# Kernel optimization log

Measured on AMD Instinct MI355X. Metric: run time of the kernel, lower is better.

## Reference

```python
import jax, jax.numpy as jnp
import numpy as np

N_NODES = 256
COND = 64
ARCH = [256, 512, 1024]
E = N_NODES * (N_NODES - 1) // 2  # 32640 upper-triangular edges
OUT = 2 * E                        # 65280 final-layer width
B = 512
CUTOFF = 0.0
TAU = 1.0


def _make_params(key, dims):
    ws, bs = [], []
    for i, (din, dout) in enumerate(zip(dims[:-1], dims[1:])):
        k = jax.random.fold_in(key, i)
        kw, kb = jax.random.split(k)
        ws.append(jax.random.normal(kw, (din, dout), jnp.float32) * 0.02)
        bs.append(jax.random.normal(kb, (dout,), jnp.float32) * 0.02)
    return ws, bs


def setup_inputs() -> dict:
    key = jax.random.key(0)
    kx, kg, kbig, ksmall = jax.random.split(key, 4)
    x = jax.random.normal(kx, (B, COND), jnp.float32)
    gumbel = jax.random.gumbel(kg, (B, E, 2), jnp.float32)
    dims = [COND] + ARCH + [OUT]
    bw, bb = _make_params(kbig, dims)
    sw, sb = _make_params(ksmall, dims)
    inp = {"x": x, "gumbel": gumbel}
    for i in range(4):
        inp[f"bw{i}"] = bw[i]; inp[f"bb{i}"] = bb[i]
        inp[f"sw{i}"] = sw[i]; inp[f"sb{i}"] = sb[i]
    return inp


def _expert_adj(x, ws, bs, gumbel):
    # MLP: relu on all but last layer
    h = x
    for w, b in zip(ws[:-1], bs[:-1]):
        h = jax.nn.relu(h @ w + b)
    logits = (h @ ws[-1] + bs[-1]).reshape(x.shape[0], E, 2)
    # hard gumbel-softmax (straight-through), tau=1
    g = (logits + gumbel) / TAU
    y_soft = jax.nn.softmax(g, axis=-1)
    y_hard = jax.nn.one_hot(jnp.argmax(g, axis=-1), 2, dtype=y_soft.dtype)
    y = y_hard + y_soft - jax.lax.stop_gradient(y_soft)
    x0 = y[:, :, 0]  # [B, E]
    iu, ju = jnp.triu_indices(N_NODES, k=1)
    adj = jnp.zeros((x.shape[0], N_NODES, N_NODES), x0.dtype)
    adj = adj.at[:, iu, ju].set(x0)
    return adj + jnp.swapaxes(adj, 1, 2)


def reference(x, gumbel,
              bw0, bb0, bw1, bb1, bw2, bb2, bw3, bb3,
              sw0, sb0, sw1, sb1, sw2, sb2, sw3, sb3):
    big_ws, big_bs = [bw0, bw1, bw2, bw3], [bb0, bb1, bb2, bb3]
    small_ws, small_bs = [sw0, sw1, sw2, sw3], [sb0, sb1, sb2, sb3]
    adj_big = _expert_adj(x, big_ws, big_bs, gumbel)
    adj_small = _expert_adj(x, small_ws, small_bs, gumbel)
    mask_big = x[:, 0] > CUTOFF  # [B]
    out = jnp.where(mask_big[:, None, None], adj_big, adj_small)
    return out
```

## Files before the change

### kernel.cpp

```cpp
#include <hip/hip_runtime.h>

#define N_NODES 256
#define COND    64
#define E_PAIRS 32640
#define OUTCOLS 65280
#define BATCH   512
#define SLOTS   576
#define D1      256
#define D2      512
#define D3      1024

typedef __attribute__((ext_vector_type(8))) short bf16x8;
typedef __attribute__((ext_vector_type(4))) float f32x4;

static __device__ __forceinline__ unsigned short f2bf(float f) {
    unsigned int u = __float_as_uint(f);
    u += 0x7FFF + ((u >> 16) & 1);
    return (unsigned short)(u >> 16);
}
static __device__ __forceinline__ float bf2f(unsigned short h) {
    return __uint_as_float(((unsigned int)h) << 16);
}

__global__ void k0_sort(const float* __restrict__ x, int* __restrict__ meta,
                        int* __restrict__ borig) {
    __shared__ int wc[9];
    int t = threadIdx.x;
    if (t < SLOTS) borig[t] = -1;
    int m = 0;
    if (t < BATCH) m = (x[t * COND] > 0.0f) ? 1 : 0;
    unsigned long long bm = __ballot(m);
    int wave = t >> 6;
    int lane = t & 63;
    int lanePre = __popcll(bm & ((1ull << lane) - 1ull));
    if (lane == 0) wc[wave] = __popcll(bm);
    __syncthreads();
    int nbig = 0, preBig = 0;
    #pragma unroll
    for (int w = 0; w < 8; ++w) {
        int c = wc[w];
        if (w < wave) preBig += c;
        nbig += c;
    }
    int S = (nbig + 63) & ~63;
    if (t < BATCH) {
        int onesBefore = preBig + lanePre;
        int slot = m ? onesBefore : (S + (t - onesBefore));
        borig[slot] = t;
    }
    if (t == 0) meta[0] = S;
}

template <bool GATHER, int K, int DOUT, bool SPLIT>
__global__ __launch_bounds__(256) void k1_gemm(
    const float* __restrict__ in,
    const float* __restrict__ wbig, const float* __restrict__ bbig,
    const float* __restrict__ wsml, const float* __restrict__ bsml,
    const int* __restrict__ meta, const int* __restrict__ borig,
    float* __restrict__ out,
    unsigned short* __restrict__ hb0, unsigned short* __restrict__ hb1,
    unsigned short* __restrict__ hb2) {
    __shared__ float hs[16][64 + 4];
    __shared__ float wt[16][64 + 4];
    int tid = threadIdx.x;
    int by = blockIdx.x;
    int bx = blockIdx.y;
    int r0 = by * 64;
    int cb = bx * 64;
    int S = meta[0];
    bool big = (r0 < S);
    const float* w = big ? wbig : wsml;
    const float* bias = big ? bbig : bsml;

    int lm = tid >> 2;
    int lq = tid & 3;
    int wk = tid >> 4;
    int wc = (tid & 15) * 4;

    int tm = tid >> 4;
    int tn = tid & 15;

    const float* hrow;
    if (GATHER) {
        int b = borig[r0 + lm];
        hrow = (b >= 0) ? &in[(size_t)b * K] : (const float*)0;
    } else {
        hrow = &in[(size_t)(r0 + lm) * K];
    }

    float acc[4][4];
    #pragma unroll
    for (int i = 0; i < 4; ++i)
        #pragma unroll
        for (int j = 0; j < 4; ++j) acc[i][j] = 0.f;

    for (int k0 = 0; k0 < K; k0 += 16) {
        float4 hv = make_float4(0.f, 0.f, 0.f, 0.f);
        if (!GATHER || hrow) hv = *(const float4*)&hrow[k0 + lq * 4];
        float4 wv = *(const float4*)&w[(size_t)(k0 + wk) * DOUT + cb + wc];
        __syncthreads();
        hs[lq * 4 + 0][lm] = hv.x;
        hs[lq * 4 + 1][lm] = hv.y;
        hs[lq * 4 + 2][lm] = hv.z;
        hs[lq * 4 + 3][lm] = hv.w;
        *(float4*)&wt[wk][wc] = wv;
        __syncthreads();
        #pragma unroll
        for (int kk = 0; kk < 16; ++kk) {
            float4 a  = *(const float4*)&hs[kk][tm * 4];
            float4 bf = *(const float4*)&wt[kk][tn * 4];
            acc[0][0] = fmaf(a.x, bf.x, acc[0][0]);
            acc[0][1] = fmaf(a.x, bf.y, acc[0][1]);
            acc[0][2] = fmaf(a.x, bf.z, acc[0][2]);
            acc[0][3] = fmaf(a.x, bf.w, acc[0][3]);
            acc[1][0] = fmaf(a.y, bf.x, acc[1][0]);
            acc[1][1] = fmaf(a.y, bf.y, acc[1][1]);
            acc[1][2] = fmaf(a.y, bf.z, acc[1][2]);
            acc[1][3] = fmaf(a.y, bf.w, acc[1][3]);
            acc[2][0] = fmaf(a.z, bf.x, acc[2][0]);
            acc[2][1] = fmaf(a.z, bf.y, acc[2][1]);
            acc[2][2] = fmaf(a.z, bf.z, acc[2][2]);
            acc[2][3] = fmaf(a.z, bf.w, acc[2][3]);
            acc[3][0] = fmaf(a.w, bf.x, acc[3][0]);
            acc[3][1] = fmaf(a.w, bf.y, acc[3][1]);
            acc[3][2] = fmaf(a.w, bf.z, acc[3][2]);
            acc[3][3] = fmaf(a.w, bf.w, acc[3][3]);
        }
    }

    float4 bv = *(const float4*)&bias[cb + tn * 4];
    #pragma unroll
    for (int i = 0; i < 4; ++i) {
        float o[4];
        o[0] = fmaxf(acc[i][0] + bv.x, 0.f);
        o[1] = fmaxf(acc[i][1] + bv.y, 0.f);
        o[2] = fmaxf(acc[i][2] + bv.z, 0.f);
        o[3] = fmaxf(acc[i][3] + bv.w, 0.f);
        size_t off = (size_t)(r0 + tm * 4 + i) * DOUT + cb + tn * 4;
        if (SPLIT) {
            ushort4 s0, s1, s2;
            unsigned short* p0[4] = {&s0.x, &s0.y, &s0.z, &s0.w};
            unsigned short* p1[4] = {&s1.x, &s1.y, &s1.z, &s1.w};
            unsigned short* p2[4] = {&s2.x, &s2.y, &s2.z, &s2.w};
            #pragma unroll
            for (int j = 0; j < 4; ++j) {
                unsigned short a0 = f2bf(o[j]);
                float r1v = o[j] - bf2f(a0);
                unsigned short a1 = f2bf(r1v);
                float r2v = r1v - bf2f(a1);
                unsigned short a2 = f2bf(r2v);
                *p0[j] = a0; *p1[j] = a1; *p2[j] = a2;
            }
            *(ushort4*)&hb0[off] = s0;
            *(ushort4*)&hb1[off] = s1;
            *(ushort4*)&hb2[off] = s2;
        } else {
            float4 ov;
            ov.x = o[0]; ov.y = o[1]; ov.z = o[2]; ov.w = o[3];
            *(float4*)&out[off] = ov;
        }
    }
}

__global__ __launch_bounds__(256) void k2_mfma(
    const unsigned short* __restrict__ hb0, const unsigned short* __restrict__ hb1,
    const unsigned short* __restrict__ hb2,
    const float* __restrict__ bw3, const float* __restrict__ bb3,
    const float* __restrict__ sw3, const float* __restrict__ sb3,
    const float* __restrict__ gum,
    const int* __restrict__ meta, const int* __restrict__ borig,
    unsigned char* __restrict__ bits) {
    __shared__ unsigned short As[3][64][32];
    __shared__ unsigned short Bs[3][128][32];

    int tid = threadIdx.x;
    int wgid = blockIdx.x;
    int xr  = wgid & 7;
    int s_  = wgid >> 3;
    int by  = s_ % 9;
    int q   = s_ / 9;
    int bx  = q * 8 + xr;
    if (bx >= 255) return;

    int r0 = by * 64;
    int cb = bx * 256;
    int db = bx * 128;
    int S = meta[0];
    bool big = (r0 < S);
    const float* w3 = big ? bw3 : sw3;
    const float* b3 = big ? bb3 : sb3;

    int lane = tid & 63;
    int wid  = tid >> 6;
    int l15  = lane & 15;
    int lg   = lane >> 4;

    int arow = tid >> 2;
    int aq   = (tid & 3) * 8;
    int bkk  = tid >> 3;
    int bc8  = tid & 7;
    int c3w  = bc8 & 3;
    int kidx = (bkk & 7) | (((bkk >> 3) ^ c3w) << 3);

    f32x4 acc[4][2];
    #pragma unroll
    for (int m = 0; m < 4; ++m)
        #pragma unroll
        for (int n = 0; n < 2; ++n) acc[m][n] = (f32x4)0.f;

    const unsigned short* ha0 = &hb0[(size_t)(r0 + arow) * D3 + aq];
    const unsigned short* ha1 = &hb1[(size_t)(r0 + arow) * D3 + aq];
    const unsigned short* ha2 = &hb2[(size_t)(r0 + arow) * D3 + aq];

    for (int k0 = 0; k0 < D3; k0 += 32) {
        uint4 av0 = *(const uint4*)&ha0[k0];
        uint4 av1 = *(const uint4*)&ha1[k0];
        uint4 av2 = *(const uint4*)&ha2[k0];
        const float* wr = &w3[(size_t)(k0 + bkk) * OUTCOLS + cb + bc8 * 32];
        float4 wv0 = *(const float4*)&wr[0];
        float4 wv1 = *(const float4*)&wr[4];
        float4 wv2 = *(const float4*)&wr[8];
        float4 wv3 = *(const float4*)&wr[12];
        float4 wv4 = *(const float4*)&wr[16];
        float4 wv5 = *(const float4*)&wr[20];
        float4 wv6 = *(const float4*)&wr[24];
        float4 wv7 = *(const float4*)&wr[28];
        __syncthreads();
        *(uint4*)&As[0][arow][aq] = av0;
        *(uint4*)&As[1][arow][aq] = av1;
        *(uint4*)&As[2][arow][aq] = av2;
        {
            float d[16] = {
                wv0.x - wv0.y, wv0.z - wv0.w, wv1.x - wv1.y, wv1.z - wv1.w,
                wv2.x - wv2.y, wv2.z - wv2.w, wv3.x - wv3.y, wv3.z - wv3.w,
                wv4.x - wv4.y, wv4.z - wv4.w, wv5.x - wv5.y, wv5.z - wv5.w,
                wv6.x - wv6.y, wv6.z - wv6.w, wv7.x - wv7.y, wv7.z - wv7.w };
            #pragma unroll
            for (int i = 0; i < 16; ++i) {
                int colv = bc8 * 16 + i;
                float dv = d[i];
                unsigned short d0 = f2bf(dv);
                float r1v = dv - bf2f(d0);
                unsigned short d1 = f2bf(r1v);
                float r2v = r1v - bf2f(d1);
                unsigned short d2 = f2bf(r2v);
                Bs[0][colv][kidx] = d0;
                Bs[1][colv][kidx] = d1;
                Bs[2][colv][kidx] = d2;
            }
        }
        __syncthreads();
        bf16x8 af0[4], af1[4], af2[4];
        #pragma unroll
        for (int m = 0; m < 4; ++m) {
            af0[m] = *(const bf16x8*)&As[0][m * 16 + l15][lg * 8];
            af1[m] = *(const bf16x8*)&As[1][m * 16 + l15][lg * 8];
            af2[m] = *(const bf16x8*)&As[2][m * 16 + l15][lg * 8];
        }
        bf16x8 bf0[2], bf1[2], bf2v[2];
        #pragma unroll
        for (int n = 0; n < 2; ++n) {
            int col = wid * 32 + n * 16 + l15;
            int kb  = (lg ^ ((col >> 4) & 3)) * 8;
            bf0[n]  = *(const bf16x8*)&Bs[0][col][kb];
            bf1[n]  = *(const bf16x8*)&Bs[1][col][kb];
            bf2v[n] = *(const bf16x8*)&Bs[2][col][kb];
        }
        #pragma unroll
        for (int m = 0; m < 4; ++m)
            #pragma unroll
            for (int n = 0; n < 2; ++n) {
                f32x4 c = acc[m][n];
                c = __builtin_amdgcn_mfma_f32_16x16x32_bf16(af0[m], bf0[n],  c, 0, 0, 0);
                c = __builtin_amdgcn_mfma_f32_16x16x32_bf16(af0[m], bf1[n],  c, 0, 0, 0);
                c = __builtin_amdgcn_mfma_f32_16x16x32_bf16(af1[m], bf0[n],  c, 0, 0, 0);
                c = __builtin_amdgcn_mfma_f32_16x16x32_bf16(af1[m], bf1[n],  c, 0, 0, 0);
                c = __builtin_amdgcn_mfma_f32_16x16x32_bf16(af0[m], bf2v[n], c, 0, 0, 0);
                c = __builtin_amdgcn_mfma_f32_16x16x32_bf16(af2[m], bf0[n],  c, 0, 0, 0);
                acc[m][n] = c;
            }
    }

    #pragma unroll
    for (int n = 0; n < 2; ++n) {
        int colg = db + wid * 32 + n * 16 + l15;
        float2 bv = *(const float2*)&b3[2 * colg];
        float bd = bv.x - bv.y;
        #pragma unroll
        for (int m = 0; m < 4; ++m) {
            #pragma unroll
            for (int r = 0; r < 4; ++r) {
                int slot = r0 + m * 16 + lg * 4 + r;
                int b = borig[slot];
                if (b < 0) continue;
                float2 gv = *(const float2*)&gum[(size_t)b * OUTCOLS + 2 * colg];
                float g = acc[m][n][r] + bd + (gv.x - gv.y);
                bits[(size_t)b * E_PAIRS + colg] = (g >= 0.f) ? 1 : 0;
            }
        }
    }
}

__global__ __launch_bounds__(256) void k3_expand(
    const unsigned char* __restrict__ bits, float* __restrict__ out) {
    __shared__ unsigned char L[64][68];
    const int ti_tab[10] = {0,0,0,0,1,1,1,2,2,3};
    const int tj_tab[10] = {0,1,2,3,1,2,3,2,3,3};
    int p = blockIdx.x;
    int b = blockIdx.y;
    int ti = ti_tab[p], tj = tj_tab[p];
    int t = threadIdx.x;

    {
        int r = t >> 2;
        int q = t & 3;
        int i = ti * 64 + r;
        long base = (long)b * E_PAIRS + (long)i * (511 - i) / 2 - i - 1;
        int j0 = tj * 64 + q * 16;
        #pragma unroll
        for (int k = 0; k < 16; ++k) {
            int j = j0 + k;
            unsigned char v = (j > i) ? bits[base + j] : (unsigned char)0;
            L[r][q * 16 + k] = v;
        }
    }
    __syncthreads();

    int h  = t >> 4;
    int w4 = (t & 15) * 4;

    {
        #pragma unroll
        for (int rr = 0; rr < 4; ++rr) {
            int ii = rr * 16 + h;
            int i_ = ti * 64 + ii;
            float4 v;
            if (ti == tj) {
                int jj;
                jj = w4 + 0; v.x = (jj > ii) ? (float)L[ii][jj] : (jj < ii ? (float)L[jj][ii] : 0.f);
                jj = w4 + 1; v.y = (jj > ii) ? (float)L[ii][jj] : (jj < ii ? (float)L[jj][ii] : 0.f);
                jj = w4 + 2; v.z = (jj > ii) ? (float)L[ii][jj] : (jj < ii ? (float)L[jj][ii] : 0.f);
                jj = w4 + 3; v.w = (jj > ii) ? (float)L[ii][jj] : (jj < ii ? (float)L[jj][ii] : 0.f);
            } else {
                v.x = (float)L[ii][w4 + 0];
                v.y = (float)L[ii][w4 + 1];
                v.z = (float)L[ii][w4 + 2];
                v.w = (float)L[ii][w4 + 3];
            }
            size_t o = (((size_t)b * 256 + i_) * 256) + tj * 64 + w4;
            *(float4*)&out[o] = v;
        }
    }

    if (ti != tj) {
        #pragma unroll
        for (int rr = 0; rr < 4; ++rr) {
            int jj = rr * 16 + h;
            int j_ = tj * 64 + jj;
            float4 v;
            v.x = (float)L[w4 + 0][jj];
            v.y = (float)L[w4 + 1][jj];
            v.z = (float)L[w4 + 2][jj];
            v.w = (float)L[w4 + 3][jj];
            size_t o = (((size_t)b * 256 + j_) * 256) + ti * 64 + w4;
            *(float4*)&out[o] = v;
        }
    }
}

extern "C" void kernel_launch(void* const* d_in, const int* in_sizes, int n_in,
                              void* d_out, int out_size, void* d_ws, size_t ws_size,
                              hipStream_t stream) {
    const float* x   = (const float*)d_in[0];
    const float* gum = (const float*)d_in[1];
    const float* bw0 = (const float*)d_in[2];  const float* bb0 = (const float*)d_in[3];
    const float* sw0 = (const float*)d_in[4];  const float* sb0 = (const float*)d_in[5];
    const float* bw1 = (const float*)d_in[6];  const float* bb1 = (const float*)d_in[7];
    const float* sw1 = (const float*)d_in[8];  const float* sb1 = (const float*)d_in[9];
    const float* bw2 = (const float*)d_in[10]; const float* bb2 = (const float*)d_in[11];
    const float* sw2 = (const float*)d_in[12]; const float* sb2 = (const float*)d_in[13];
    const float* bw3 = (const float*)d_in[14]; const float* bb3 = (const float*)d_in[15];
    const float* sw3 = (const float*)d_in[16]; const float* sb3 = (const float*)d_in[17];

    char* ws = (char*)d_ws;
    int*   meta  = (int*)ws;
    int*   borig = (int*)(ws + 64);
    float* act1  = (float*)(ws + 4096);
    float* act2  = (float*)(ws + 593920);
    unsigned short* hb0 = (unsigned short*)(ws + 1773568);
    unsigned short* hb1 = (unsigned short*)(ws + 2953216);
    unsigned short* hb2 = (unsigned short*)(ws + 4132864);
    unsigned char* bits = (unsigned char*)(ws + 5312512);
    float* out = (float*)d_out;

    k0_sort<<<1, SLOTS, 0, stream>>>(x, meta, borig);
    k1_gemm<true,  COND, D1, false><<<dim3(9, D1 / 64), 256, 0, stream>>>(
        x,    bw0, bb0, sw0, sb0, meta, borig, act1, 0, 0, 0);
    k1_gemm<false, D1,   D2, false><<<dim3(9, D2 / 64), 256, 0, stream>>>(
        act1, bw1, bb1, sw1, sb1, meta, borig, act2, 0, 0, 0);
    k1_gemm<false, D2,   D3, true><<<dim3(9, D3 / 64), 256, 0, stream>>>(
        act2, bw2, bb2, sw2, sb2, meta, borig, (float*)0, hb0, hb1, hb2);
    k2_mfma<<<2304, 256, 0, stream>>>(hb0, hb1, hb2, bw3, bb3, sw3, sb3, gum,
                                      meta, borig, bits);
    k3_expand<<<dim3(10, BATCH), 256, 0, stream>>>(bits, out);
}
```

Before: 1.050 ms.

## Pre-swizzle activation limbs into MFMA fragment layout and drop LDS staging

The layer-3 output is now written by the split GEMM directly in an MFMA-fragment-ordered layout, with the three bf16 limbs interleaved per k-tile. The final-layer MFMA kernel can then load A fragments straight from global memory. B fragments are built in registers from direct strided weight loads, so all shared memory and __syncthreads are removed. This removes LDS traffic and barriers, but each wave now rereads the weight column data itself and issues uncoalesced float2 loads strided by OUTCOLS. Launch bounds also request 2 blocks per SM.

Result: faster. 1.020 ms (-2.8%).

```diff
diff --git a/kernel.cpp b/kernel.cpp
--- a/kernel.cpp
+++ b/kernel.cpp
@@ -12,6 +12,7 @@
 
 typedef __attribute__((ext_vector_type(8))) short bf16x8;
 typedef __attribute__((ext_vector_type(4))) float f32x4;
+typedef __attribute__((ext_vector_type(4))) unsigned int u32x4;
 
 static __device__ __forceinline__ unsigned short f2bf(float f) {
     unsigned int u = __float_as_uint(f);
@@ -57,9 +58,7 @@
     const float* __restrict__ wbig, const float* __restrict__ bbig,
     const float* __restrict__ wsml, const float* __restrict__ bsml,
     const int* __restrict__ meta, const int* __restrict__ borig,
-    float* __restrict__ out,
-    unsigned short* __restrict__ hb0, unsigned short* __restrict__ hb1,
-    unsigned short* __restrict__ hb2) {
+    float* __restrict__ out, unsigned short* __restrict__ hbA) {
     __shared__ float hs[16][64 + 4];
     __shared__ float wt[16][64 + 4];
     int tid = threadIdx.x;
@@ -136,43 +135,44 @@
         o[1] = fmaxf(acc[i][1] + bv.y, 0.f);
         o[2] = fmaxf(acc[i][2] + bv.z, 0.f);
         o[3] = fmaxf(acc[i][3] + bv.w, 0.f);
-        size_t off = (size_t)(r0 + tm * 4 + i) * DOUT + cb + tn * 4;
         if (SPLIT) {
+            int row = r0 + tm * 4 + i;
+            int by_ = row >> 6, rl = row & 63;
+            int mfr = rl >> 4, p15 = rl & 15;
+            int kt  = cb + tn * 4;
+            int kk  = kt >> 5, lgk = (kt >> 3) & 3, j0 = kt & 7;
+            size_t base = (size_t)(by_ * 32 + kk) * 6144 + (size_t)mfr * 512
+                        + (size_t)(lgk * 16 + p15) * 8 + j0;
             ushort4 s0, s1, s2;
-            unsigned short* p0[4] = {&s0.x, &s0.y, &s0.z, &s0.w};
-            unsigned short* p1[4] = {&s1.x, &s1.y, &s1.z, &s1.w};
-            unsigned short* p2[4] = {&s2.x, &s2.y, &s2.z, &s2.w};
+            unsigned short* q0[4] = {&s0.x, &s0.y, &s0.z, &s0.w};
+            unsigned short* q1[4] = {&s1.x, &s1.y, &s1.z, &s1.w};
+            unsigned short* q2[4] = {&s2.x, &s2.y, &s2.z, &s2.w};
             #pragma unroll
             for (int j = 0; j < 4; ++j) {
                 unsigned short a0 = f2bf(o[j]);
                 float r1v = o[j] - bf2f(a0);
                 unsigned short a1 = f2bf(r1v);
                 float r2v = r1v - bf2f(a1);
-                unsigned short a2 = f2bf(r2v);
-                *p0[j] = a0; *p1[j] = a1; *p2[j] = a2;
-            }
-            *(ushort4*)&hb0[off] = s0;
-            *(ushort4*)&hb1[off] = s1;
-            *(ushort4*)&hb2[off] = s2;
+                *q0[j] = a0; *q1[j] = a1; *q2[j] = f2bf(r2v);
+            }
+            *(ushort4*)&hbA[base]        = s0;
+            *(ushort4*)&hbA[base + 2048] = s1;
+            *(ushort4*)&hbA[base + 4096] = s2;
         } else {
             float4 ov;
             ov.x = o[0]; ov.y = o[1]; ov.z = o[2]; ov.w = o[3];
-            *(float4*)&out[off] = ov;
-        }
-    }
-}
-
-__global__ __launch_bounds__(256) void k2_mfma(
-    const unsigned short* __restrict__ hb0, const unsigned short* __restrict__ hb1,
-    const unsigned short* __restrict__ hb2,
+            *(float4*)&out[(size_t)(r0 + tm * 4 + i) * DOUT + cb + tn * 4] = ov;
+        }
+    }
+}
+
+__global__ __launch_bounds__(256, 2) void k2_mfma(
+    const unsigned short* __restrict__ hbA,
     const float* __restrict__ bw3, const float* __restrict__ bb3,
     const float* __restrict__ sw3, const float* __restrict__ sb3,
     const float* __restrict__ gum,
     const int* __restrict__ meta, const int* __restrict__ borig,
     unsigned char* __restrict__ bits) {
-    __shared__ unsigned short As[3][64][32];
-    __shared__ unsigned short Bs[3][128][32];
-
     int tid = threadIdx.x;
     int wgid = blockIdx.x;
     int xr  = wgid & 7;
@@ -183,7 +183,6 @@
     if (bx >= 255) return;
 
     int r0 = by * 64;
-    int cb = bx * 256;
     int db = bx * 128;
     int S = meta[0];
     bool big = (r0 < S);
@@ -195,12 +194,7 @@
     int l15  = lane & 15;
     int lg   = lane >> 4;
 
-    int arow = tid >> 2;
-    int aq   = (tid & 3) * 8;
-    int bkk  = tid >> 3;
-    int bc8  = tid & 7;
-    int c3w  = bc8 & 3;
-    int kidx = (bkk & 7) | (((bkk >> 3) ^ c3w) << 3);
+    int colg0 = db + wid * 32 + l15;
 
     f32x4 acc[4][2];
     #pragma unroll
@@ -208,77 +202,58 @@
         #pragma unroll
         for (int n = 0; n < 2; ++n) acc[m][n] = (f32x4)0.f;
 
-    const unsigned short* ha0 = &hb0[(size_t)(r0 + arow) * D3 + aq];
-    const unsigned short* ha1 = &hb1[(size_t)(r0 + arow) * D3 + aq];
-    const unsigned short* ha2 = &hb2[(size_t)(r0 + arow) * D3 + aq];
-
-    for (int k0 = 0; k0 < D3; k0 += 32) {
-        uint4 av0 = *(const uint4*)&ha0[k0];
-        uint4 av1 = *(const uint4*)&ha1[k0];
-        uint4 av2 = *(const uint4*)&ha2[k0];
-        const float* wr = &w3[(size_t)(k0 + bkk) * OUTCOLS + cb + bc8 * 32];
-        float4 wv0 = *(const float4*)&wr[0];
-        float4 wv1 = *(const float4*)&wr[4];
-        float4 wv2 = *(const float4*)&wr[8];
-        float4 wv3 = *(const float4*)&wr[12];
-        float4 wv4 = *(const float4*)&wr[16];
-        float4 wv5 = *(const float4*)&wr[20];
-        float4 wv6 = *(const float4*)&wr[24];
-        float4 wv7 = *(const float4*)&wr[28];
-        __syncthreads();
-        *(uint4*)&As[0][arow][aq] = av0;
-        *(uint4*)&As[1][arow][aq] = av1;
-        *(uint4*)&As[2][arow][aq] = av2;
-        {
-            float d[16] = {
-                wv0.x - wv0.y, wv0.z - wv0.w, wv1.x - wv1.y, wv1.z - wv1.w,
-                wv2.x - wv2.y, wv2.z - wv2.w, wv3.x - wv3.y, wv3.z - wv3.w,
-                wv4.x - wv4.y, wv4.z - wv4.w, wv5.x - wv5.y, wv5.z - wv5.w,
-                wv6.x - wv6.y, wv6.z - wv6.w, wv7.x - wv7.y, wv7.z - wv7.w };
-            #pragma unroll
-            for (int i = 0; i < 16; ++i) {
-                int colv = bc8 * 16 + i;
-                float dv = d[i];
-                unsigned short d0 = f2bf(dv);
-                float r1v = dv - bf2f(d0);
-                unsigned short d1 = f2bf(r1v);
-                float r2v = r1v - bf2f(d1);
-                unsigned short d2 = f2bf(r2v);
-                Bs[0][colv][kidx] = d0;
-                Bs[1][colv][kidx] = d1;
-                Bs[2][colv][kidx] = d2;
-            }
-        }
-        __syncthreads();
-        bf16x8 af0[4], af1[4], af2[4];
-        #pragma unroll
-        for (int m = 0; m < 4; ++m) {
-            af0[m] = *(const bf16x8*)&As[0][m * 16 + l15][lg * 8];
-            af1[m] = *(const bf16x8*)&As[1][m * 16 + l15][lg * 8];
-            af2[m] = *(const bf16x8*)&As[2][m * 16 + l15][lg * 8];
-        }
-        bf16x8 bf0[2], bf1[2], bf2v[2];
+    const unsigned short* ap0 = hbA + (size_t)(by * 32) * 6144 + (size_t)lane * 8;
+
+    for (int kk = 0; kk < 32; ++kk) {
+        const unsigned short* ap = ap0 + (size_t)kk * 6144;
+        bf16x8 af[3][4];
+        #pragma unroll
+        for (int limb = 0; limb < 3; ++limb)
+            #pragma unroll
+            for (int m = 0; m < 4; ++m)
+                af[limb][m] = *(const bf16x8*)(ap + limb * 2048 + m * 512);
+
+        u32x4 fr0[2], fr1[2], fr2[2];
         #pragma unroll
         for (int n = 0; n < 2; ++n) {
-            int col = wid * 32 + n * 16 + l15;
-            int kb  = (lg ^ ((col >> 4) & 3)) * 8;
-            bf0[n]  = *(const bf16x8*)&Bs[0][col][kb];
-            bf1[n]  = *(const bf16x8*)&Bs[1][col][kb];
-            bf2v[n] = *(const bf16x8*)&Bs[2][col][kb];
-        }
-        #pragma unroll
-        for (int m = 0; m < 4; ++m)
-            #pragma unroll
-            for (int n = 0; n < 2; ++n) {
+            const float* wp = w3 + (size_t)(kk * 32 + lg * 8) * OUTCOLS
+                                 + 2 * (colg0 + n * 16);
+            float d[8];
+            #pragma unroll
+            for (int j = 0; j < 8; ++j) {
+                float2 v = *(const float2*)(wp + (size_t)j * OUTCOLS);
+                d[j] = v.x - v.y;
+            }
+            #pragma unroll
+            for (int w = 0; w < 4; ++w) {
+                float dA = d[2 * w], dB = d[2 * w + 1];
+                unsigned short aL = f2bf(dA), aH = f2bf(dB);
+                fr0[n][w] = (unsigned int)aL | ((unsigned int)aH << 16);
+                float rA = dA - bf2f(aL), rB = dB - bf2f(aH);
+                unsigned short bL = f2bf(rA), bH = f2bf(rB);
+                fr1[n][w] = (unsigned int)bL | ((unsigned int)bH << 16);
+                float sA = rA - bf2f(bL), sB = rB - bf2f(bH);
+                fr2[n][w] = (unsigned int)f2bf(sA) | ((unsigned int)f2bf(sB) << 16);
+            }
+        }
+
+        #pragma unroll
+        for (int n = 0; n < 2; ++n) {
+            bf16x8 b0 = __builtin_bit_cast(bf16x8, fr0[n]);
+            bf16x8 b1 = __builtin_bit_cast(bf16x8, fr1[n]);
+            bf16x8 b2 = __builtin_bit_cast(bf16x8, fr2[n]);
+            #pragma unroll
+            for (int m = 0; m < 4; ++m) {
                 f32x4 c = acc[m][n];
-                c = __builtin_amdgcn_mfma_f32_16x16x32_bf16(af0[m], bf0[n],  c, 0, 0, 0);
-                c = __builtin_amdgcn_mfma_f32_16x16x32_bf16(af0[m], bf1[n],  c, 0, 0, 0);
-                c = __builtin_amdgcn_mfma_f32_16x16x32_bf16(af1[m], bf0[n],  c, 0, 0, 0);
-                c = __builtin_amdgcn_mfma_f32_16x16x32_bf16(af1[m], bf1[n],  c, 0, 0, 0);
-                c = __builtin_amdgcn_mfma_f32_16x16x32_bf16(af0[m], bf2v[n], c, 0, 0, 0);
-                c = __builtin_amdgcn_mfma_f32_16x16x32_bf16(af2[m], bf0[n],  c, 0, 0, 0);
+                c = __builtin_amdgcn_mfma_f32_16x16x32_bf16(af[0][m], b0, c, 0, 0, 0);
+                c = __builtin_amdgcn_mfma_f32_16x16x32_bf16(af[0][m], b1, c, 0, 0, 0);
+                c = __builtin_amdgcn_mfma_f32_16x16x32_bf16(af[1][m], b0, c, 0, 0, 0);
+                c = __builtin_amdgcn_mfma_f32_16x16x32_bf16(af[1][m], b1, c, 0, 0, 0);
+                c = __builtin_amdgcn_mfma_f32_16x16x32_bf16(af[0][m], b2, c, 0, 0, 0);
+                c = __builtin_amdgcn_mfma_f32_16x16x32_bf16(af[2][m], b0, c, 0, 0, 0);
                 acc[m][n] = c;
             }
+        }
     }
 
     #pragma unroll
@@ -387,20 +362,18 @@
     int*   borig = (int*)(ws + 64);
     float* act1  = (float*)(ws + 4096);
     float* act2  = (float*)(ws + 593920);
-    unsigned short* hb0 = (unsigned short*)(ws + 1773568);
-    unsigned short* hb1 = (unsigned short*)(ws + 2953216);
-    unsigned short* hb2 = (unsigned short*)(ws + 4132864);
+    unsigned short* hbA = (unsigned short*)(ws + 1773568);
     unsigned char* bits = (unsigned char*)(ws + 5312512);
     float* out = (float*)d_out;
 
     k0_sort<<<1, SLOTS, 0, stream>>>(x, meta, borig);
     k1_gemm<true,  COND, D1, false><<<dim3(9, D1 / 64), 256, 0, stream>>>(
-        x,    bw0, bb0, sw0, sb0, meta, borig, act1, 0, 0, 0);
+        x,    bw0, bb0, sw0, sb0, meta, borig, act1, 0);
     k1_gemm<false, D1,   D2, false><<<dim3(9, D2 / 64), 256, 0, stream>>>(
-        act1, bw1, bb1, sw1, sb1, meta, borig, act2, 0, 0, 0);
+        act1, bw1, bb1, sw1, sb1, meta, borig, act2, 0);
     k1_gemm<false, D2,   D3, true><<<dim3(9, D3 / 64), 256, 0, stream>>>(
-        act2, bw2, bb2, sw2, sb2, meta, borig, (float*)0, hb0, hb1, hb2);
-    k2_mfma<<<2304, 256, 0, stream>>>(hb0, hb1, hb2, bw3, bb3, sw3, sb3, gum,
+        act2, bw2, bb2, sw2, sb2, meta, borig, (float*)0, hbA);
+    k2_mfma<<<2304, 256, 0, stream>>>(hbA, bw3, bb3, sw3, sb3, gum,
                                       meta, borig, bits);
     k3_expand<<<dim3(10, BATCH), 256, 0, stream>>>(bits, out);
 }
```
